# Performance work log

Measured on AMD Instinct MI355X. Metric: run time of the kernel, lower is better.

The kernel has to match this reference:

```python
import jax, jax.numpy as jnp
import numpy as np

B, NF, NI = 4, 8, 1
C_ASPP = 512
H32, W32 = 32, 32
H8, W8 = 128, 128
C = C_ASPP // 16  # 32 channels after PixelShuffle(4)
D = 32 * 4 + 4 * 1 + 4 + 1  # 137 dynamic-kernel params per instance
BN_EPS = 1e-5


def pixel_shuffle(x, r):
    # torch PixelShuffle: out[n, c, h*r+i, w*r+j] = in[n, c*r*r + i*r + j, h, w]
    n, cr2, h, w = x.shape
    c = cr2 // (r * r)
    x = x.reshape(n, c, r, r, h, w)
    x = x.transpose(0, 1, 4, 2, 5, 3)
    return x.reshape(n, c, h * r, w * r)


def conv2d(x, w, b, pad):
    y = jax.lax.conv_general_dilated(
        x, w, window_strides=(1, 1), padding=[(pad, pad), (pad, pad)],
        dimension_numbers=("NCHW", "OIHW", "NCHW"))
    return y + b[None, :, None, None]


def setup_inputs() -> dict:
    key = jax.random.key(0)
    ks = jax.random.split(key, 6)
    return {
        "embedding": jax.random.normal(ks[0], (B * NF, C_ASPP, H32, W32), jnp.float32),
        "inc_kernels": jax.random.normal(ks[1], (B, NF, NI, D), jnp.float32) * 0.1,
        "coarse_masks": jax.random.uniform(ks[2], (B, NF, NI, H8, W8), dtype=jnp.float32),
        "conv_w": jax.random.normal(ks[3], (C, C, 3, 3), jnp.float32) * 0.05,
        "conv_b": jnp.zeros((C,), jnp.float32),
        "bn_gamma": jnp.ones((C,), jnp.float32),
        "bn_beta": jnp.zeros((C,), jnp.float32),
        "bn_mean": jnp.zeros((C,), jnp.float32),
        "bn_var": jnp.ones((C,), jnp.float32),
        "smooth_w": jax.random.normal(ks[4], (1, 2, 5, 5), jnp.float32) * 0.05,
        "smooth_b": jnp.zeros((1,), jnp.float32),
    }


def reference(embedding, inc_kernels, coarse_masks, conv_w, conv_b,
              bn_gamma, bn_beta, bn_mean, bn_var, smooth_w, smooth_b):
    # inc_conv: PixelShuffle(4) -> Conv3x3 -> BatchNorm(eval) -> ReLU
    x = pixel_shuffle(embedding, 4)              # (B*NF, 32, 128, 128)
    x = conv2d(x, conv_w, conv_b, 1)
    scale = (bn_gamma / jnp.sqrt(bn_var + BN_EPS))[None, :, None, None]
    x = (x - bn_mean[None, :, None, None]) * scale + bn_beta[None, :, None, None]
    x = jax.nn.relu(x)

    # per-instance dynamic 1x1 convs (groups = B*NF*NI; NI=1 so each frame is a group)
    G = B * NF * NI
    k = inc_kernels.reshape(G, D)
    w1 = k[:, :128].reshape(G, 4, 32)            # layer1: 32 -> 4
    w2 = k[:, 128:132].reshape(G, 1, 4)          # layer2: 4 -> 1
    b1 = k[:, 132:136]
    b2 = k[:, 136:137]

    hfeat = jax.nn.relu(jnp.einsum('goc,gchw->gohw', w1, x) + b1[:, :, None, None])
    y = jnp.einsum('goc,gchw->gohw', w2, hfeat) + b2[:, :, None, None]  # (G,1,H8,W8)

    m = coarse_masks.reshape(G, 1, H8, W8)
    z = jnp.concatenate([jax.nn.sigmoid(y), m], axis=1)  # (G, 2, H8, W8)
    z = conv2d(z, smooth_w, smooth_b, 2)                 # inc_smooth 5x5
    return z.reshape(B * NF, NI, H8, W8)
```

## Files before the change

kernel.cpp:

```cpp
#include <hip/hip_runtime.h>


typedef __attribute__((ext_vector_type(8))) short short8;
typedef __attribute__((ext_vector_type(4))) float f32x4;

static __device__ __forceinline__ ushort f2bf(float x) {
    union { float f; uint u; } v; v.f = x;
    uint r = v.u + 0x7fffu + ((v.u >> 16) & 1u);
    return (ushort)(r >> 16);
}
static __device__ __forceinline__ uint cvt_pk_bf16(float lo, float hi) {
    uint r;
    asm("v_cvt_pk_bf16_f32 %0, %1, %2" : "=v"(r) : "v"(lo), "v"(hi));
    return r;
}

#define SIG_ELEMS (32 * 128 * 128)
#define BFRAG_OFF (SIG_ELEMS * 4)
#define SH_OFF    (BFRAG_OFF + 18432)
#define HDP_OFF   (SH_OFF + 128)

__global__ void prep_kernel(const float* __restrict__ conv_w,
                            const float* __restrict__ conv_b,
                            const float* __restrict__ bn_gamma,
                            const float* __restrict__ bn_beta,
                            const float* __restrict__ bn_mean,
                            const float* __restrict__ bn_var,
                            const float* __restrict__ inc,
                            ushort* __restrict__ bfrag,
                            float* __restrict__ shb,
                            float* __restrict__ hdp) {
    int t = blockIdx.x * 256 + threadIdx.x;
    if (t < 9216) {
        int j    = t & 7;
        int lane = (t >> 3) & 63;
        int knt  = t >> 9;
        int kk   = knt >> 1;
        int nt   = knt & 1;
        int oc   = (lane & 15) + nt * 16;
        int c    = (lane >> 4) * 8 + j;
        float sc = bn_gamma[oc] * rsqrtf(bn_var[oc] + 1e-5f);
        bfrag[t] = f2bf(conv_w[oc * 288 + c * 9 + kk] * sc);
    } else if (t < 9248) {
        int oc = t - 9216;
        float sc = bn_gamma[oc] * rsqrtf(bn_var[oc] + 1e-5f);
        shb[oc] = (conv_b[oc] - bn_mean[oc]) * sc + bn_beta[oc];
    } else if (t < 9248 + 32 * 137) {
        int i = t - 9248;
        int nn = i / 137, r = i - nn * 137;
        hdp[nn * 144 + r] = inc[i];
    }
}

#define PITCHB 8320

__global__ __launch_bounds__(256, 4) void fused_main_kernel(
    const float* __restrict__ emb,
    const ushort* __restrict__ bfrag,
    const float* __restrict__ shb,
    const float* __restrict__ hdp,
    float* __restrict__ sig_out)
{
    __shared__ __align__(16) char smem[4 * PITCHB];

    const int bid = blockIdx.x;
    const int lid = (bid & 7) * 256 + (bid >> 3);
    const int n    = lid >> 6;
    const int band = lid & 63;
    const int h0   = band << 1;

    const int tid  = threadIdx.x;

    const int f    = tid & 7;
    const int cphi = (tid >> 3) & 3;
    const int sx   = (tid >> 5) & 3;
    const int yA   = tid >> 7;
    const int yB   = yA + 2;
    const int hA   = h0 + yA - 1;
    const int hB   = h0 + yB - 1;
    const bool vA  = (unsigned)hA < 128u;
    const bool vB  = (unsigned)hB < 128u;

    float4 pA0[4], pA1[4], pB0[4], pB1[4];
    #pragma unroll
    for (int cplo = 0; cplo < 4; ++cplo) {
        pA0[cplo] = make_float4(0.f, 0.f, 0.f, 0.f);
        pA1[cplo] = pA0[cplo]; pB0[cplo] = pA0[cplo]; pB1[cplo] = pA0[cplo];
        if (vA) {
            int cc = cphi * 128 + cplo * 32 + ((hA & 3) << 2) + sx;
            long base = ((long)(n * 512 + cc) << 10) + ((hA >> 2) << 5) + (f << 2);
            pA0[cplo] = *reinterpret_cast<const float4*>(&emb[base]);
            pA1[cplo] = *reinterpret_cast<const float4*>(&emb[base + (16 << 10)]);
        }
        if (vB) {
            int cc = cphi * 128 + cplo * 32 + ((hB & 3) << 2) + sx;
            long base = ((long)(n * 512 + cc) << 10) + ((hB >> 2) << 5) + (f << 2);
            pB0[cplo] = *reinterpret_cast<const float4*>(&emb[base]);
            pB1[cplo] = *reinterpret_cast<const float4*>(&emb[base + (16 << 10)]);
        }
    }
    __builtin_amdgcn_sched_barrier(0);

    if (tid < 128) {
        int y   = tid >> 5;
        int col = (tid >> 4) & 1;
        int wrd = tid & 15;
        ((uint*)smem)[(y * PITCHB + (col ? 129 : 0) * 64) / 4 + wrd] = 0u;
    }

    #pragma unroll
    for (int e = 0; e < 4; ++e) {
        int xi   = 1 + sx + (f << 4) + (e << 2);
        int slot = (cphi ^ ((xi >> 1) ^ (xi >> 4))) & 3;
        int off  = xi * 64 + (slot << 4);
        const float a00[4] = {pA0[0].x, pA0[0].y, pA0[0].z, pA0[0].w};
        const float a01[4] = {pA0[1].x, pA0[1].y, pA0[1].z, pA0[1].w};
        const float a02[4] = {pA0[2].x, pA0[2].y, pA0[2].z, pA0[2].w};
        const float a03[4] = {pA0[3].x, pA0[3].y, pA0[3].z, pA0[3].w};
        const float a10[4] = {pA1[0].x, pA1[0].y, pA1[0].z, pA1[0].w};
        const float a11[4] = {pA1[1].x, pA1[1].y, pA1[1].z, pA1[1].w};
        const float a12[4] = {pA1[2].x, pA1[2].y, pA1[2].z, pA1[2].w};
        const float a13[4] = {pA1[3].x, pA1[3].y, pA1[3].z, pA1[3].w};
        uint4 qa;
        qa.x = cvt_pk_bf16(a00[e], a10[e]);
        qa.y = cvt_pk_bf16(a01[e], a11[e]);
        qa.z = cvt_pk_bf16(a02[e], a12[e]);
        qa.w = cvt_pk_bf16(a03[e], a13[e]);
        *reinterpret_cast<uint4*>(&smem[yA * PITCHB + off]) = qa;
        const float b00[4] = {pB0[0].x, pB0[0].y, pB0[0].z, pB0[0].w};
        const float b01[4] = {pB0[1].x, pB0[1].y, pB0[1].z, pB0[1].w};
        const float b02[4] = {pB0[2].x, pB0[2].y, pB0[2].z, pB0[2].w};
        const float b03[4] = {pB0[3].x, pB0[3].y, pB0[3].z, pB0[3].w};
        const float b10[4] = {pB1[0].x, pB1[0].y, pB1[0].z, pB1[0].w};
        const float b11[4] = {pB1[1].x, pB1[1].y, pB1[1].z, pB1[1].w};
        const float b12[4] = {pB1[2].x, pB1[2].y, pB1[2].z, pB1[2].w};
        const float b13[4] = {pB1[3].x, pB1[3].y, pB1[3].z, pB1[3].w};
        uint4 qb;
        qb.x = cvt_pk_bf16(b00[e], b10[e]);
        qb.y = cvt_pk_bf16(b01[e], b11[e]);
        qb.z = cvt_pk_bf16(b02[e], b12[e]);
        qb.w = cvt_pk_bf16(b03[e], b13[e]);
        *reinterpret_cast<uint4*>(&smem[yB * PITCHB + off]) = qb;
    }
    __syncthreads();

    const int lane = tid & 63;
    const int wv   = tid >> 6;
    const int g    = lane >> 4;
    const int m    = lane & 15;
    const int rw   = wv >> 1;
    const int xq   = (wv & 1) * 64;

    int adr[4][3];
    #pragma unroll
    for (int t = 0; t < 4; ++t)
        #pragma unroll
        for (int dx = 0; dx < 3; ++dx) {
            int xi = xq + t * 16 + m + dx;
            int slot = (g ^ ((xi >> 1) ^ (xi >> 4))) & 3;
            adr[t][dx] = rw * PITCHB + xi * 64 + (slot << 4);
        }

    f32x4 acc[4][2];
    #pragma unroll
    for (int t = 0; t < 4; ++t)
        #pragma unroll
        for (int nt = 0; nt < 2; ++nt)
            acc[t][nt] = (f32x4){0.f, 0.f, 0.f, 0.f};

    #pragma unroll
    for (int kk = 0; kk < 9; ++kk) {
        const int dy = kk / 3, dxs = kk % 3;
        short8 b0 = *reinterpret_cast<const short8*>(bfrag + (((kk * 2 + 0) * 64 + lane) << 3));
        short8 b1 = *reinterpret_cast<const short8*>(bfrag + (((kk * 2 + 1) * 64 + lane) << 3));
        #pragma unroll
        for (int t = 0; t < 4; ++t) {
            short8 a = *reinterpret_cast<const short8*>(&smem[adr[t][dxs] + dy * PITCHB]);
            acc[t][0] = __builtin_amdgcn_mfma_f32_16x16x32_bf16(b0, a, acc[t][0], 0, 0, 0);
            acc[t][1] = __builtin_amdgcn_mfma_f32_16x16x32_bf16(b1, a, acc[t][1], 0, 0, 0);
        }
    }

    const float* hd = hdp + n * 144;
    const f32x4 shA = *reinterpret_cast<const f32x4*>(&shb[g * 4]);
    const f32x4 shB = *reinterpret_cast<const f32x4*>(&shb[16 + g * 4]);
    f32x4 w1A[4], w1B[4];
    #pragma unroll
    for (int o = 0; o < 4; ++o) {
        w1A[o] = *reinterpret_cast<const f32x4*>(&hd[o * 32 + g * 4]);
        w1B[o] = *reinterpret_cast<const f32x4*>(&hd[o * 32 + 16 + g * 4]);
    }

    float ph[4][4];
    #pragma unroll
    for (int t = 0; t < 4; ++t) {
        f32x4 vA, vB;
        vA.x = fmaxf(acc[t][0].x + shA.x, 0.f);
        vA.y = fmaxf(acc[t][0].y + shA.y, 0.f);
        vA.z = fmaxf(acc[t][0].z + shA.z, 0.f);
        vA.w = fmaxf(acc[t][0].w + shA.w, 0.f);
        vB.x = fmaxf(acc[t][1].x + shB.x, 0.f);
        vB.y = fmaxf(acc[t][1].y + shB.y, 0.f);
        vB.z = fmaxf(acc[t][1].z + shB.z, 0.f);
        vB.w = fmaxf(acc[t][1].w + shB.w, 0.f);
        #pragma unroll
        for (int o = 0; o < 4; ++o) {
            float p = vA.x * w1A[o].x;
            p = fmaf(vA.y, w1A[o].y, p);
            p = fmaf(vA.z, w1A[o].z, p);
            p = fmaf(vA.w, w1A[o].w, p);
            p = fmaf(vB.x, w1B[o].x, p);
            p = fmaf(vB.y, w1B[o].y, p);
            p = fmaf(vB.z, w1B[o].z, p);
            p = fmaf(vB.w, w1B[o].w, p);
            ph[t][o] = p;
        }
    }
    #pragma unroll
    for (int t = 0; t < 4; ++t)
        #pragma unroll
        for (int o = 0; o < 4; ++o) {
            float s = ph[t][o];
            s += __shfl_xor(s, 16);
            s += __shfl_xor(s, 32);
            ph[t][o] = s;
        }

    const f32x4 w2v = *reinterpret_cast<const f32x4*>(&hd[128]);
    const f32x4 b1v = *reinterpret_cast<const f32x4*>(&hd[132]);
    const float b2  = hd[136];
    float yv[4];
    #pragma unroll
    for (int t = 0; t < 4; ++t) {
        float q0 = fmaxf(ph[t][0] + b1v.x, 0.f);
        float q1 = fmaxf(ph[t][1] + b1v.y, 0.f);
        float q2 = fmaxf(ph[t][2] + b1v.z, 0.f);
        float q3 = fmaxf(ph[t][3] + b1v.w, 0.f);
        float yy = b2;
        yy = fmaf(w2v.x, q0, yy);
        yy = fmaf(w2v.y, q1, yy);
        yy = fmaf(w2v.z, q2, yy);
        yy = fmaf(w2v.w, q3, yy);
        yv[t] = yy;
    }
    float ysel = (g == 0) ? yv[0] : (g == 1) ? yv[1] : (g == 2) ? yv[2] : yv[3];
    float s = 1.0f / (1.0f + __expf(-ysel));
    sig_out[(n << 14) + ((h0 + rw) << 7) + xq + lane] = s;
}

__global__ __launch_bounds__(256) void smooth_kernel(
    const float* __restrict__ sig,
    const float* __restrict__ masks,
    const float* __restrict__ sw,
    const float* __restrict__ sb,
    float* __restrict__ out)
{
    __shared__ float ls[2][400];

    const int tid  = threadIdx.x;
    const int n    = blockIdx.x >> 6;
    const int tile = blockIdx.x & 63;
    const int h0   = (tile >> 3) << 4;
    const int w0   = (tile & 7) << 4;

    for (int i = tid; i < 800; i += 256) {
        int chn = (i >= 400) ? 1 : 0;
        int r  = i - chn * 400;
        int yy = r / 20;
        int xx = r - yy * 20;
        int h  = h0 + yy - 2;
        int w  = w0 + xx - 2;
        float v = 0.0f;
        if ((unsigned)h < 128u && (unsigned)w < 128u) {
            const float* src = chn ? masks : sig;
            v = src[(n << 14) + (h << 7) + w];
        }
        ls[chn][r] = v;
    }
    __syncthreads();

    const int tx = tid & 15;
    const int ty = tid >> 4;

    float accv = sb[0];
    #pragma unroll
    for (int chn = 0; chn < 2; ++chn)
        #pragma unroll
        for (int dy = 0; dy < 5; ++dy)
            #pragma unroll
            for (int dx = 0; dx < 5; ++dx)
                accv = fmaf(ls[chn][(ty + dy) * 20 + tx + dx],
                            sw[(chn * 5 + dy) * 5 + dx], accv);
    out[(n << 14) + ((h0 + ty) << 7) + (w0 + tx)] = accv;
}

extern "C" void kernel_launch(void* const* d_in, const int* in_sizes, int n_in,
                              void* d_out, int out_size, void* d_ws, size_t ws_size,
                              hipStream_t stream) {
    const float* emb     = (const float*)d_in[0];
    const float* inc     = (const float*)d_in[1];
    const float* masks   = (const float*)d_in[2];
    const float* conv_w  = (const float*)d_in[3];
    const float* conv_b  = (const float*)d_in[4];
    const float* bn_g    = (const float*)d_in[5];
    const float* bn_b    = (const float*)d_in[6];
    const float* bn_m    = (const float*)d_in[7];
    const float* bn_v    = (const float*)d_in[8];
    const float* sw      = (const float*)d_in[9];
    const float* sb      = (const float*)d_in[10];
    float*  out   = (float*)d_out;
    float*  sig   = (float*)d_ws;
    ushort* bfrag = (ushort*)((char*)d_ws + BFRAG_OFF);
    float*  shb   = (float*)((char*)d_ws + SH_OFF);
    float*  hdp   = (float*)((char*)d_ws + HDP_OFF);

    prep_kernel<<<54, 256, 0, stream>>>(conv_w, conv_b, bn_g, bn_b, bn_m, bn_v,
                                        inc, bfrag, shb, hdp);
    fused_main_kernel<<<2048, 256, 0, stream>>>(emb, bfrag, shb, hdp, sig);
    smooth_kernel<<<2048, 256, 0, stream>>>(sig, masks, sw, sb, out);
}
```

Before: 36.61 us.

## Process 8-row bands per block with a ring buffer and prefetched input rows

Each block of the fused conv kernel now covers 8 output rows instead of 2, looping 4 times over a 6-row LDS ring buffer. This cuts the redundant halo reloads of the embedding. The next two input rows are loaded from global memory while the current MFMA pass runs, then written into the ring afterwards. The grid shrinks to 512 blocks, LDS per block grows, and the occupancy hint drops to 2 blocks. That means fewer resident waves to hide latency, and a sync after each iteration.

```diff
diff --git a/kernel.cpp b/kernel.cpp
--- a/kernel.cpp
+++ b/kernel.cpp
@@ -53,66 +53,61 @@
 }
 
 #define PITCHB 8320
-
-__global__ __launch_bounds__(256, 4) void fused_main_kernel(
+#define NRING  6
+
+__global__ __launch_bounds__(256, 2) void fused_main_kernel(
     const float* __restrict__ emb,
     const ushort* __restrict__ bfrag,
     const float* __restrict__ shb,
     const float* __restrict__ hdp,
     float* __restrict__ sig_out)
 {
-    __shared__ __align__(16) char smem[4 * PITCHB];
+    __shared__ __align__(16) char smem[NRING * PITCHB];
 
     const int bid = blockIdx.x;
-    const int lid = (bid & 7) * 256 + (bid >> 3);
-    const int n    = lid >> 6;
-    const int band = lid & 63;
-    const int h0   = band << 1;
+    const int lid = (bid & 7) * 64 + (bid >> 3);
+    const int n   = lid >> 4;
+    const int q   = lid & 15;
+    const int hq0 = q << 3;
 
     const int tid  = threadIdx.x;
 
     const int f    = tid & 7;
     const int cphi = (tid >> 3) & 3;
     const int sx   = (tid >> 5) & 3;
-    const int yA   = tid >> 7;
-    const int yB   = yA + 2;
-    const int hA   = h0 + yA - 1;
-    const int hB   = h0 + yB - 1;
-    const bool vA  = (unsigned)hA < 128u;
-    const bool vB  = (unsigned)hB < 128u;
-
-    float4 pA0[4], pA1[4], pB0[4], pB1[4];
-    #pragma unroll
-    for (int cplo = 0; cplo < 4; ++cplo) {
-        pA0[cplo] = make_float4(0.f, 0.f, 0.f, 0.f);
-        pA1[cplo] = pA0[cplo]; pB0[cplo] = pA0[cplo]; pB1[cplo] = pA0[cplo];
-        if (vA) {
-            int cc = cphi * 128 + cplo * 32 + ((hA & 3) << 2) + sx;
-            long base = ((long)(n * 512 + cc) << 10) + ((hA >> 2) << 5) + (f << 2);
-            pA0[cplo] = *reinterpret_cast<const float4*>(&emb[base]);
-            pA1[cplo] = *reinterpret_cast<const float4*>(&emb[base + (16 << 10)]);
-        }
-        if (vB) {
-            int cc = cphi * 128 + cplo * 32 + ((hB & 3) << 2) + sx;
-            long base = ((long)(n * 512 + cc) << 10) + ((hB >> 2) << 5) + (f << 2);
-            pB0[cplo] = *reinterpret_cast<const float4*>(&emb[base]);
-            pB1[cplo] = *reinterpret_cast<const float4*>(&emb[base + (16 << 10)]);
-        }
-    }
-    __builtin_amdgcn_sched_barrier(0);
-
-    if (tid < 128) {
-        int y   = tid >> 5;
-        int col = (tid >> 4) & 1;
-        int wrd = tid & 15;
-        ((uint*)smem)[(y * PITCHB + (col ? 129 : 0) * 64) / 4 + wrd] = 0u;
-    }
-
-    #pragma unroll
-    for (int e = 0; e < 4; ++e) {
-        int xi   = 1 + sx + (f << 4) + (e << 2);
-        int slot = (cphi ^ ((xi >> 1) ^ (xi >> 4))) & 3;
-        int off  = xi * 64 + (slot << 4);
+    const int yy   = tid >> 7;
+
+    {
+        const int rA = yy, rB = yy + 2;
+        const int hA = hq0 + rA - 1, hB = hq0 + rB - 1;
+        const bool vA = (unsigned)hA < 128u;
+        const bool vB = (unsigned)hB < 128u;
+        float4 pA0[4], pA1[4], pB0[4], pB1[4];
+        #pragma unroll
+        for (int cplo = 0; cplo < 4; ++cplo) {
+            pA0[cplo] = make_float4(0.f, 0.f, 0.f, 0.f);
+            pA1[cplo] = pA0[cplo]; pB0[cplo] = pA0[cplo]; pB1[cplo] = pA0[cplo];
+            if (vA) {
+                int cc = cphi * 128 + cplo * 32 + ((hA & 3) << 2) + sx;
+                long base = ((long)(n * 512 + cc) << 10) + ((hA >> 2) << 5) + (f << 2);
+                pA0[cplo] = *reinterpret_cast<const float4*>(&emb[base]);
+                pA1[cplo] = *reinterpret_cast<const float4*>(&emb[base + (16 << 10)]);
+            }
+            if (vB) {
+                int cc = cphi * 128 + cplo * 32 + ((hB & 3) << 2) + sx;
+                long base = ((long)(n * 512 + cc) << 10) + ((hB >> 2) << 5) + (f << 2);
+                pB0[cplo] = *reinterpret_cast<const float4*>(&emb[base]);
+                pB1[cplo] = *reinterpret_cast<const float4*>(&emb[base + (16 << 10)]);
+            }
+        }
+        __builtin_amdgcn_sched_barrier(0);
+        if (tid < 192) {
+            int cell = tid >> 4;
+            int wrd  = tid & 15;
+            int row  = cell >> 1;
+            int col  = (cell & 1) ? 129 : 0;
+            ((uint*)smem)[(row * PITCHB + col * 64) / 4 + wrd] = 0u;
+        }
         const float a00[4] = {pA0[0].x, pA0[0].y, pA0[0].z, pA0[0].w};
         const float a01[4] = {pA0[1].x, pA0[1].y, pA0[1].z, pA0[1].w};
         const float a02[4] = {pA0[2].x, pA0[2].y, pA0[2].z, pA0[2].w};
@@ -121,12 +116,6 @@
         const float a11[4] = {pA1[1].x, pA1[1].y, pA1[1].z, pA1[1].w};
         const float a12[4] = {pA1[2].x, pA1[2].y, pA1[2].z, pA1[2].w};
         const float a13[4] = {pA1[3].x, pA1[3].y, pA1[3].z, pA1[3].w};
-        uint4 qa;
-        qa.x = cvt_pk_bf16(a00[e], a10[e]);
-        qa.y = cvt_pk_bf16(a01[e], a11[e]);
-        qa.z = cvt_pk_bf16(a02[e], a12[e]);
-        qa.w = cvt_pk_bf16(a03[e], a13[e]);
-        *reinterpret_cast<uint4*>(&smem[yA * PITCHB + off]) = qa;
         const float b00[4] = {pB0[0].x, pB0[0].y, pB0[0].z, pB0[0].w};
         const float b01[4] = {pB0[1].x, pB0[1].y, pB0[1].z, pB0[1].w};
         const float b02[4] = {pB0[2].x, pB0[2].y, pB0[2].z, pB0[2].w};
@@ -135,14 +124,25 @@
         const float b11[4] = {pB1[1].x, pB1[1].y, pB1[1].z, pB1[1].w};
         const float b12[4] = {pB1[2].x, pB1[2].y, pB1[2].z, pB1[2].w};
         const float b13[4] = {pB1[3].x, pB1[3].y, pB1[3].z, pB1[3].w};
-        uint4 qb;
-        qb.x = cvt_pk_bf16(b00[e], b10[e]);
-        qb.y = cvt_pk_bf16(b01[e], b11[e]);
-        qb.z = cvt_pk_bf16(b02[e], b12[e]);
-        qb.w = cvt_pk_bf16(b03[e], b13[e]);
-        *reinterpret_cast<uint4*>(&smem[yB * PITCHB + off]) = qb;
-    }
-    __syncthreads();
+        #pragma unroll
+        for (int e = 0; e < 4; ++e) {
+            int xi   = 1 + sx + (f << 4) + (e << 2);
+            int slot = (cphi ^ ((xi >> 1) ^ (xi >> 4))) & 3;
+            int off  = xi * 64 + (slot << 4);
+            uint4 qa;
+            qa.x = cvt_pk_bf16(a00[e], a10[e]);
+            qa.y = cvt_pk_bf16(a01[e], a11[e]);
+            qa.z = cvt_pk_bf16(a02[e], a12[e]);
+            qa.w = cvt_pk_bf16(a03[e], a13[e]);
+            *reinterpret_cast<uint4*>(&smem[rA * PITCHB + off]) = qa;
+            uint4 qb;
+            qb.x = cvt_pk_bf16(b00[e], b10[e]);
+            qb.y = cvt_pk_bf16(b01[e], b11[e]);
+            qb.z = cvt_pk_bf16(b02[e], b12[e]);
+            qb.w = cvt_pk_bf16(b03[e], b13[e]);
+            *reinterpret_cast<uint4*>(&smem[rB * PITCHB + off]) = qb;
+        }
+    }
 
     const int lane = tid & 63;
     const int wv   = tid >> 6;
@@ -151,35 +151,15 @@
     const int rw   = wv >> 1;
     const int xq   = (wv & 1) * 64;
 
-    int adr[4][3];
+    int cell_off[4][3];
     #pragma unroll
     for (int t = 0; t < 4; ++t)
         #pragma unroll
         for (int dx = 0; dx < 3; ++dx) {
             int xi = xq + t * 16 + m + dx;
             int slot = (g ^ ((xi >> 1) ^ (xi >> 4))) & 3;
-            adr[t][dx] = rw * PITCHB + xi * 64 + (slot << 4);
-        }
-
-    f32x4 acc[4][2];
-    #pragma unroll
-    for (int t = 0; t < 4; ++t)
-        #pragma unroll
-        for (int nt = 0; nt < 2; ++nt)
-            acc[t][nt] = (f32x4){0.f, 0.f, 0.f, 0.f};
-
-    #pragma unroll
-    for (int kk = 0; kk < 9; ++kk) {
-        const int dy = kk / 3, dxs = kk % 3;
-        short8 b0 = *reinterpret_cast<const short8*>(bfrag + (((kk * 2 + 0) * 64 + lane) << 3));
-        short8 b1 = *reinterpret_cast<const short8*>(bfrag + (((kk * 2 + 1) * 64 + lane) << 3));
-        #pragma unroll
-        for (int t = 0; t < 4; ++t) {
-            short8 a = *reinterpret_cast<const short8*>(&smem[adr[t][dxs] + dy * PITCHB]);
-            acc[t][0] = __builtin_amdgcn_mfma_f32_16x16x32_bf16(b0, a, acc[t][0], 0, 0, 0);
-            acc[t][1] = __builtin_amdgcn_mfma_f32_16x16x32_bf16(b1, a, acc[t][1], 0, 0, 0);
-        }
-    }
+            cell_off[t][dx] = xi * 64 + (slot << 4);
+        }
 
     const float* hd = hdp + n * 144;
     const f32x4 shA = *reinterpret_cast<const f32x4*>(&shb[g * 4]);
@@ -190,62 +170,136 @@
         w1A[o] = *reinterpret_cast<const f32x4*>(&hd[o * 32 + g * 4]);
         w1B[o] = *reinterpret_cast<const f32x4*>(&hd[o * 32 + 16 + g * 4]);
     }
-
-    float ph[4][4];
-    #pragma unroll
-    for (int t = 0; t < 4; ++t) {
-        f32x4 vA, vB;
-        vA.x = fmaxf(acc[t][0].x + shA.x, 0.f);
-        vA.y = fmaxf(acc[t][0].y + shA.y, 0.f);
-        vA.z = fmaxf(acc[t][0].z + shA.z, 0.f);
-        vA.w = fmaxf(acc[t][0].w + shA.w, 0.f);
-        vB.x = fmaxf(acc[t][1].x + shB.x, 0.f);
-        vB.y = fmaxf(acc[t][1].y + shB.y, 0.f);
-        vB.z = fmaxf(acc[t][1].z + shB.z, 0.f);
-        vB.w = fmaxf(acc[t][1].w + shB.w, 0.f);
-        #pragma unroll
-        for (int o = 0; o < 4; ++o) {
-            float p = vA.x * w1A[o].x;
-            p = fmaf(vA.y, w1A[o].y, p);
-            p = fmaf(vA.z, w1A[o].z, p);
-            p = fmaf(vA.w, w1A[o].w, p);
-            p = fmaf(vB.x, w1B[o].x, p);
-            p = fmaf(vB.y, w1B[o].y, p);
-            p = fmaf(vB.z, w1B[o].z, p);
-            p = fmaf(vB.w, w1B[o].w, p);
-            ph[t][o] = p;
-        }
-    }
-    #pragma unroll
-    for (int t = 0; t < 4; ++t)
-        #pragma unroll
-        for (int o = 0; o < 4; ++o) {
-            float s = ph[t][o];
-            s += __shfl_xor(s, 16);
-            s += __shfl_xor(s, 32);
-            ph[t][o] = s;
-        }
-
     const f32x4 w2v = *reinterpret_cast<const f32x4*>(&hd[128]);
     const f32x4 b1v = *reinterpret_cast<const f32x4*>(&hd[132]);
     const float b2  = hd[136];
-    float yv[4];
-    #pragma unroll
-    for (int t = 0; t < 4; ++t) {
-        float q0 = fmaxf(ph[t][0] + b1v.x, 0.f);
-        float q1 = fmaxf(ph[t][1] + b1v.y, 0.f);
-        float q2 = fmaxf(ph[t][2] + b1v.z, 0.f);
-        float q3 = fmaxf(ph[t][3] + b1v.w, 0.f);
-        float yy = b2;
-        yy = fmaf(w2v.x, q0, yy);
-        yy = fmaf(w2v.y, q1, yy);
-        yy = fmaf(w2v.z, q2, yy);
-        yy = fmaf(w2v.w, q3, yy);
-        yv[t] = yy;
-    }
-    float ysel = (g == 0) ? yv[0] : (g == 1) ? yv[1] : (g == 2) ? yv[2] : yv[3];
-    float s = 1.0f / (1.0f + __expf(-ysel));
-    sig_out[(n << 14) + ((h0 + rw) << 7) + xq + lane] = s;
+
+    __syncthreads();
+
+    #pragma unroll 1
+    for (int it = 0; it < 4; ++it) {
+        float4 np0[4], np1[4];
+        const bool have = (it < 3);
+        const int  hn   = hq0 + 2 * it + 3 + yy;
+        const bool vn   = have && (hn < 128);
+        #pragma unroll
+        for (int cplo = 0; cplo < 4; ++cplo) {
+            np0[cplo] = make_float4(0.f, 0.f, 0.f, 0.f);
+            np1[cplo] = np0[cplo];
+            if (vn) {
+                int cc = cphi * 128 + cplo * 32 + ((hn & 3) << 2) + sx;
+                long base = ((long)(n * 512 + cc) << 10) + ((hn >> 2) << 5) + (f << 2);
+                np0[cplo] = *reinterpret_cast<const float4*>(&emb[base]);
+                np1[cplo] = *reinterpret_cast<const float4*>(&emb[base + (16 << 10)]);
+            }
+        }
+        __builtin_amdgcn_sched_barrier(0);
+
+        int rb[3];
+        #pragma unroll
+        for (int dy = 0; dy < 3; ++dy) {
+            int r = 2 * it + rw + dy;
+            if (r >= NRING) r -= NRING;
+            rb[dy] = r * PITCHB;
+        }
+
+        f32x4 acc[4][2];
+        #pragma unroll
+        for (int t = 0; t < 4; ++t)
+            #pragma unroll
+            for (int nt = 0; nt < 2; ++nt)
+                acc[t][nt] = (f32x4){0.f, 0.f, 0.f, 0.f};
+
+        #pragma unroll
+        for (int kk = 0; kk < 9; ++kk) {
+            const int dy = kk / 3, dxs = kk % 3;
+            short8 b0 = *reinterpret_cast<const short8*>(bfrag + (((kk * 2 + 0) * 64 + lane) << 3));
+            short8 b1 = *reinterpret_cast<const short8*>(bfrag + (((kk * 2 + 1) * 64 + lane) << 3));
+            #pragma unroll
+            for (int t = 0; t < 4; ++t) {
+                short8 a = *reinterpret_cast<const short8*>(&smem[rb[dy] + cell_off[t][dxs]]);
+                acc[t][0] = __builtin_amdgcn_mfma_f32_16x16x32_bf16(b0, a, acc[t][0], 0, 0, 0);
+                acc[t][1] = __builtin_amdgcn_mfma_f32_16x16x32_bf16(b1, a, acc[t][1], 0, 0, 0);
+            }
+        }
+
+        float ph[4][4];
+        #pragma unroll
+        for (int t = 0; t < 4; ++t) {
+            f32x4 vA, vB;
+            vA.x = fmaxf(acc[t][0].x + shA.x, 0.f);
+            vA.y = fmaxf(acc[t][0].y + shA.y, 0.f);
+            vA.z = fmaxf(acc[t][0].z + shA.z, 0.f);
+            vA.w = fmaxf(acc[t][0].w + shA.w, 0.f);
+            vB.x = fmaxf(acc[t][1].x + shB.x, 0.f);
+            vB.y = fmaxf(acc[t][1].y + shB.y, 0.f);
+            vB.z = fmaxf(acc[t][1].z + shB.z, 0.f);
+            vB.w = fmaxf(acc[t][1].w + shB.w, 0.f);
+            #pragma unroll
+            for (int o = 0; o < 4; ++o) {
+                float p = vA.x * w1A[o].x;
+                p = fmaf(vA.y, w1A[o].y, p);
+                p = fmaf(vA.z, w1A[o].z, p);
+                p = fmaf(vA.w, w1A[o].w, p);
+                p = fmaf(vB.x, w1B[o].x, p);
+                p = fmaf(vB.y, w1B[o].y, p);
+                p = fmaf(vB.z, w1B[o].z, p);
+                p = fmaf(vB.w, w1B[o].w, p);
+                ph[t][o] = p;
+            }
+        }
+        #pragma unroll
+        for (int t = 0; t < 4; ++t)
+            #pragma unroll
+            for (int o = 0; o < 4; ++o) {
+                float s = ph[t][o];
+                s += __shfl_xor(s, 16);
+                s += __shfl_xor(s, 32);
+                ph[t][o] = s;
+            }
+        float yv[4];
+        #pragma unroll
+        for (int t = 0; t < 4; ++t) {
+            float q0 = fmaxf(ph[t][0] + b1v.x, 0.f);
+            float q1 = fmaxf(ph[t][1] + b1v.y, 0.f);
+            float q2 = fmaxf(ph[t][2] + b1v.z, 0.f);
+            float q3 = fmaxf(ph[t][3] + b1v.w, 0.f);
+            float yyv = b2;
+            yyv = fmaf(w2v.x, q0, yyv);
+            yyv = fmaf(w2v.y, q1, yyv);
+            yyv = fmaf(w2v.z, q2, yyv);
+            yyv = fmaf(w2v.w, q3, yyv);
+            yv[t] = yyv;
+        }
+        float ysel = (g == 0) ? yv[0] : (g == 1) ? yv[1] : (g == 2) ? yv[2] : yv[3];
+        float sv = 1.0f / (1.0f + __expf(-ysel));
+        sig_out[(n << 14) + ((hq0 + 2 * it + rw) << 7) + xq + lane] = sv;
+
+        if (have) {
+            int rs = 2 * it + 4 + yy;
+            if (rs >= NRING) rs -= NRING;
+            const float c00[4] = {np0[0].x, np0[0].y, np0[0].z, np0[0].w};
+            const float c01[4] = {np0[1].x, np0[1].y, np0[1].z, np0[1].w};
+            const float c02[4] = {np0[2].x, np0[2].y, np0[2].z, np0[2].w};
+            const float c03[4] = {np0[3].x, np0[3].y, np0[3].z, np0[3].w};
+            const float c10[4] = {np1[0].x, np1[0].y, np1[0].z, np1[0].w};
+            const float c11[4] = {np1[1].x, np1[1].y, np1[1].z, np1[1].w};
+            const float c12[4] = {np1[2].x, np1[2].y, np1[2].z, np1[2].w};
+            const float c13[4] = {np1[3].x, np1[3].y, np1[3].z, np1[3].w};
+            #pragma unroll
+            for (int e = 0; e < 4; ++e) {
+                int xi   = 1 + sx + (f << 4) + (e << 2);
+                int slot = (cphi ^ ((xi >> 1) ^ (xi >> 4))) & 3;
+                uint4 qv;
+                qv.x = cvt_pk_bf16(c00[e], c10[e]);
+                qv.y = cvt_pk_bf16(c01[e], c11[e]);
+                qv.z = cvt_pk_bf16(c02[e], c12[e]);
+                qv.w = cvt_pk_bf16(c03[e], c13[e]);
+                *reinterpret_cast<uint4*>(&smem[rs * PITCHB + xi * 64 + (slot << 4)]) = qv;
+            }
+        }
+        __syncthreads();
+    }
 }
 
 __global__ __launch_bounds__(256) void smooth_kernel(
@@ -316,6 +370,6 @@
 
     prep_kernel<<<54, 256, 0, stream>>>(conv_w, conv_b, bn_g, bn_b, bn_m, bn_v,
                                         inc, bfrag, shb, hdp);
-    fused_main_kernel<<<2048, 256, 0, stream>>>(emb, bfrag, shb, hdp, sig);
+    fused_main_kernel<<<512, 256, 0, stream>>>(emb, bfrag, shb, hdp, sig);
     smooth_kernel<<<2048, 256, 0, stream>>>(sig, masks, sw, sb, out);
 }
```

Measured after the change: 35.82 us. -2.1%, faster.

## Remap load thread indexing, raise MFMA priority, use butterfly transpose-reduce epilogue

Applied to the files above, without the earlier changes.

Reorders the thread-to-data mapping for the embedding loads so sx and cphi vary fastest within a wave, which changes global-load coalescing and LDS store patterns. Wraps the MFMA loop in s_setprio to favour matrix issue over other waves. Replaces the 32-shuffle all-reduce plus per-lane select in the epilogue with a transpose-reduce butterfly that needs 12 shuffles and computes only the lane's own tile. This cuts cross-lane traffic and ALU work, but the new load mapping may fetch fewer contiguous bytes per instruction.

```diff
diff --git a/kernel.cpp b/kernel.cpp
--- a/kernel.cpp
+++ b/kernel.cpp
@@ -71,16 +71,15 @@
 
     const int tid  = threadIdx.x;
 
-    const int f    = tid & 7;
-    const int cphi = (tid >> 3) & 3;
-    const int sx   = (tid >> 5) & 3;
-    const int yA   = tid >> 7;
-    const int yB   = yA + 2;
-    const int hA   = h0 + yA - 1;
-    const int hB   = h0 + yB - 1;
-    const bool vA  = (unsigned)hA < 128u;
-    const bool vB  = (unsigned)hB < 128u;
-
+    const int sx   = tid & 3;
+    const int cphi = (tid >> 2) & 3;
+    const int f    = (tid >> 4) & 7;
+    const int yy   = tid >> 7;
+
+    const int rA = yy, rB = yy + 2;
+    const int hA = h0 + rA - 1, hB = h0 + rB - 1;
+    const bool vA = (unsigned)hA < 128u;
+    const bool vB = (unsigned)hB < 128u;
     float4 pA0[4], pA1[4], pB0[4], pB1[4];
     #pragma unroll
     for (int cplo = 0; cplo < 4; ++cplo) {
@@ -108,11 +107,7 @@
         ((uint*)smem)[(y * PITCHB + (col ? 129 : 0) * 64) / 4 + wrd] = 0u;
     }
 
-    #pragma unroll
-    for (int e = 0; e < 4; ++e) {
-        int xi   = 1 + sx + (f << 4) + (e << 2);
-        int slot = (cphi ^ ((xi >> 1) ^ (xi >> 4))) & 3;
-        int off  = xi * 64 + (slot << 4);
+    {
         const float a00[4] = {pA0[0].x, pA0[0].y, pA0[0].z, pA0[0].w};
         const float a01[4] = {pA0[1].x, pA0[1].y, pA0[1].z, pA0[1].w};
         const float a02[4] = {pA0[2].x, pA0[2].y, pA0[2].z, pA0[2].w};
@@ -121,12 +116,6 @@
         const float a11[4] = {pA1[1].x, pA1[1].y, pA1[1].z, pA1[1].w};
         const float a12[4] = {pA1[2].x, pA1[2].y, pA1[2].z, pA1[2].w};
         const float a13[4] = {pA1[3].x, pA1[3].y, pA1[3].z, pA1[3].w};
-        uint4 qa;
-        qa.x = cvt_pk_bf16(a00[e], a10[e]);
-        qa.y = cvt_pk_bf16(a01[e], a11[e]);
-        qa.z = cvt_pk_bf16(a02[e], a12[e]);
-        qa.w = cvt_pk_bf16(a03[e], a13[e]);
-        *reinterpret_cast<uint4*>(&smem[yA * PITCHB + off]) = qa;
         const float b00[4] = {pB0[0].x, pB0[0].y, pB0[0].z, pB0[0].w};
         const float b01[4] = {pB0[1].x, pB0[1].y, pB0[1].z, pB0[1].w};
         const float b02[4] = {pB0[2].x, pB0[2].y, pB0[2].z, pB0[2].w};
@@ -135,12 +124,24 @@
         const float b11[4] = {pB1[1].x, pB1[1].y, pB1[1].z, pB1[1].w};
         const float b12[4] = {pB1[2].x, pB1[2].y, pB1[2].z, pB1[2].w};
         const float b13[4] = {pB1[3].x, pB1[3].y, pB1[3].z, pB1[3].w};
-        uint4 qb;
-        qb.x = cvt_pk_bf16(b00[e], b10[e]);
-        qb.y = cvt_pk_bf16(b01[e], b11[e]);
-        qb.z = cvt_pk_bf16(b02[e], b12[e]);
-        qb.w = cvt_pk_bf16(b03[e], b13[e]);
-        *reinterpret_cast<uint4*>(&smem[yB * PITCHB + off]) = qb;
+        #pragma unroll
+        for (int e = 0; e < 4; ++e) {
+            int xi   = 1 + sx + (f << 4) + (e << 2);
+            int slot = (cphi ^ ((xi >> 1) ^ (xi >> 4))) & 3;
+            int off  = xi * 64 + (slot << 4);
+            uint4 qa;
+            qa.x = cvt_pk_bf16(a00[e], a10[e]);
+            qa.y = cvt_pk_bf16(a01[e], a11[e]);
+            qa.z = cvt_pk_bf16(a02[e], a12[e]);
+            qa.w = cvt_pk_bf16(a03[e], a13[e]);
+            *reinterpret_cast<uint4*>(&smem[rA * PITCHB + off]) = qa;
+            uint4 qb;
+            qb.x = cvt_pk_bf16(b00[e], b10[e]);
+            qb.y = cvt_pk_bf16(b01[e], b11[e]);
+            qb.z = cvt_pk_bf16(b02[e], b12[e]);
+            qb.w = cvt_pk_bf16(b03[e], b13[e]);
+            *reinterpret_cast<uint4*>(&smem[rB * PITCHB + off]) = qb;
+        }
     }
     __syncthreads();
 
@@ -150,15 +151,17 @@
     const int m    = lane & 15;
     const int rw   = wv >> 1;
     const int xq   = (wv & 1) * 64;
-
-    int adr[4][3];
+    const int gb0  = g & 1;
+    const int gb1  = (g >> 1) & 1;
+
+    int cell_off[4][3];
     #pragma unroll
     for (int t = 0; t < 4; ++t)
         #pragma unroll
         for (int dx = 0; dx < 3; ++dx) {
             int xi = xq + t * 16 + m + dx;
             int slot = (g ^ ((xi >> 1) ^ (xi >> 4))) & 3;
-            adr[t][dx] = rw * PITCHB + xi * 64 + (slot << 4);
+            cell_off[t][dx] = rw * PITCHB + xi * 64 + (slot << 4);
         }
 
     f32x4 acc[4][2];
@@ -168,6 +171,7 @@
         for (int nt = 0; nt < 2; ++nt)
             acc[t][nt] = (f32x4){0.f, 0.f, 0.f, 0.f};
 
+    __builtin_amdgcn_s_setprio(1);
     #pragma unroll
     for (int kk = 0; kk < 9; ++kk) {
         const int dy = kk / 3, dxs = kk % 3;
@@ -175,11 +179,12 @@
         short8 b1 = *reinterpret_cast<const short8*>(bfrag + (((kk * 2 + 1) * 64 + lane) << 3));
         #pragma unroll
         for (int t = 0; t < 4; ++t) {
-            short8 a = *reinterpret_cast<const short8*>(&smem[adr[t][dxs] + dy * PITCHB]);
+            short8 a = *reinterpret_cast<const short8*>(&smem[cell_off[t][dxs] + dy * PITCHB]);
             acc[t][0] = __builtin_amdgcn_mfma_f32_16x16x32_bf16(b0, a, acc[t][0], 0, 0, 0);
             acc[t][1] = __builtin_amdgcn_mfma_f32_16x16x32_bf16(b1, a, acc[t][1], 0, 0, 0);
         }
     }
+    __builtin_amdgcn_s_setprio(0);
 
     const float* hd = hdp + n * 144;
     const f32x4 shA = *reinterpret_cast<const f32x4*>(&shb[g * 4]);
@@ -190,6 +195,9 @@
         w1A[o] = *reinterpret_cast<const f32x4*>(&hd[o * 32 + g * 4]);
         w1B[o] = *reinterpret_cast<const f32x4*>(&hd[o * 32 + 16 + g * 4]);
     }
+    const f32x4 w2v = *reinterpret_cast<const f32x4*>(&hd[128]);
+    const f32x4 b1v = *reinterpret_cast<const f32x4*>(&hd[132]);
+    const float b2  = hd[136];
 
     float ph[4][4];
     #pragma unroll
@@ -216,36 +224,35 @@
             ph[t][o] = p;
         }
     }
-    #pragma unroll
-    for (int t = 0; t < 4; ++t)
-        #pragma unroll
-        for (int o = 0; o < 4; ++o) {
-            float s = ph[t][o];
-            s += __shfl_xor(s, 16);
-            s += __shfl_xor(s, 32);
-            ph[t][o] = s;
-        }
-
-    const f32x4 w2v = *reinterpret_cast<const f32x4*>(&hd[128]);
-    const f32x4 b1v = *reinterpret_cast<const f32x4*>(&hd[132]);
-    const float b2  = hd[136];
-    float yv[4];
-    #pragma unroll
-    for (int t = 0; t < 4; ++t) {
-        float q0 = fmaxf(ph[t][0] + b1v.x, 0.f);
-        float q1 = fmaxf(ph[t][1] + b1v.y, 0.f);
-        float q2 = fmaxf(ph[t][2] + b1v.z, 0.f);
-        float q3 = fmaxf(ph[t][3] + b1v.w, 0.f);
-        float yy = b2;
-        yy = fmaf(w2v.x, q0, yy);
-        yy = fmaf(w2v.y, q1, yy);
-        yy = fmaf(w2v.z, q2, yy);
-        yy = fmaf(w2v.w, q3, yy);
-        yv[t] = yy;
-    }
-    float ysel = (g == 0) ? yv[0] : (g == 1) ? yv[1] : (g == 2) ? yv[2] : yv[3];
-    float s = 1.0f / (1.0f + __expf(-ysel));
-    sig_out[(n << 14) + ((h0 + rw) << 7) + xq + lane] = s;
+
+    float k0[4], k1[4], tot[4];
+    #pragma unroll
+    for (int o = 0; o < 4; ++o) {
+        float send0 = gb0 ? ph[0][o] : ph[1][o];
+        float r0 = __shfl_xor(send0, 16);
+        k0[o] = (gb0 ? ph[1][o] : ph[0][o]) + r0;
+        float send1 = gb0 ? ph[2][o] : ph[3][o];
+        float r1 = __shfl_xor(send1, 16);
+        k1[o] = (gb0 ? ph[3][o] : ph[2][o]) + r1;
+    }
+    #pragma unroll
+    for (int o = 0; o < 4; ++o) {
+        float send = gb1 ? k0[o] : k1[o];
+        float r = __shfl_xor(send, 32);
+        tot[o] = (gb1 ? k1[o] : k0[o]) + r;
+    }
+
+    float q0 = fmaxf(tot[0] + b1v.x, 0.f);
+    float q1 = fmaxf(tot[1] + b1v.y, 0.f);
+    float q2 = fmaxf(tot[2] + b1v.z, 0.f);
+    float q3 = fmaxf(tot[3] + b1v.w, 0.f);
+    float yv = b2;
+    yv = fmaf(w2v.x, q0, yv);
+    yv = fmaf(w2v.y, q1, yv);
+    yv = fmaf(w2v.z, q2, yv);
+    yv = fmaf(w2v.w, q3, yv);
+    float sv = 1.0f / (1.0f + __expf(-yv));
+    sig_out[(n << 14) + ((h0 + rw) << 7) + xq + lane] = sv;
 }
 
 __global__ __launch_bounds__(256) void smooth_kernel(
```

After: 41.30 us. 12.8% more time.
